# Performance work log

Hardware: AMD Instinct MI355X
Metric: run time of the kernel (lower is better)

## Reference

```python
import jax, jax.numpy as jnp
import numpy as np

GROUPS = 4
EPS = 1e-5


def conv1d(x, w, b):
    # x [B,Cin,NA,T], w [Cout,Cin,1,K], 'same' padding along T
    K = w.shape[-1]
    pad = (K - 1) // 2
    y = jax.lax.conv_general_dilated(x, w, (1, 1), [(0, 0), (pad, pad)],
                                     dimension_numbers=('NCHW', 'OIHW', 'NCHW'))
    return y + b[None, :, None, None]


def group_norm(x, g, b):
    B, C, H, W = x.shape
    xg = x.reshape(B, GROUPS, C // GROUPS, H, W)
    m = xg.mean((2, 3, 4), keepdims=True)
    v = xg.var((2, 3, 4), keepdims=True)
    xn = ((xg - m) * jax.lax.rsqrt(v + EPS)).reshape(B, C, H, W)
    return xn * g[None, :, None, None] + b[None, :, None, None]


def avg_pool_t(x, k):
    B, C, H, T = x.shape
    return x.reshape(B, C, H, T // k, k).mean(-1)


def branch(x, w1, b1, g1, be1, w2, b2, g2, be2):
    y = avg_pool_t(jax.nn.gelu(group_norm(conv1d(x, w1, b1), g1, be1), approximate=False), 2)
    y = avg_pool_t(jax.nn.gelu(group_norm(conv1d(y, w2, b2), g2, be2), approximate=False), 4)
    # B C NA T -> B NA (T C)
    B, C, NA, T = y.shape
    return jnp.transpose(y, (0, 2, 3, 1)).reshape(B, NA, T * C)


def rvq(feat, cbs):
    # feat [B,NA,D]; cbs [nq,V,D] -> residual vector quantization
    def step(res, cb):
        d = (res * res).sum(-1, keepdims=True) \
            - 2.0 * jnp.einsum('bnd,vd->bnv', res, cb) \
            + (cb * cb).sum(-1)              # [B,NA,V]
        idx = jnp.argmin(d, axis=-1)          # [B,NA]
        q = cb[idx]                           # gather [B,NA,D]
        return res - q, (q, idx)
    _, (qs, idxs) = jax.lax.scan(step, feat, cbs)
    return qs.sum(0), idxs                    # [B,NA,D], [nq,B,NA]


def reference(x, w11, w12, w13, w14, b1, g1, be1,
              w21, w22, w23, w24, b2, g2, be2, codebooks):
    B, N, A, T = x.shape
    xc = x.reshape(B, N * A, T)[:, None]  # [B,1,NA,T]
    feats = jnp.stack([
        branch(xc, w11, b1[0], g1[0], be1[0], w21, b2[0], g2[0], be2[0]),
        branch(xc, w12, b1[1], g1[1], be1[1], w22, b2[1], g2[1], be2[1]),
        branch(xc, w13, b1[2], g1[2], be1[2], w23, b2[2], g2[2], be2[2]),
        branch(xc, w14, b1[3], g1[3], be1[3], w24, b2[3], g2[3], be2[3]),
    ])  # [4,B,NA,D]
    quant, idxs = jax.vmap(rvq)(feats, codebooks)  # [4,B,NA,D], [4,nq,B,NA]
    # straight-through estimator
    out = feats + jax.lax.stop_gradient(quant - feats)
    return out, idxs


def setup_inputs() -> dict:
    key = jax.random.key(0)
    ks = jax.random.split(key, 16)
    C = 8
    d = {
        'x': jax.random.normal(ks[0], (8, 32, 4, 200), jnp.float32),
        'w11': jax.random.normal(ks[1], (C, 1, 1, 21), jnp.float32) * 0.1,
        'w12': jax.random.normal(ks[2], (C, 1, 1, 15), jnp.float32) * 0.1,
        'w13': jax.random.normal(ks[3], (C, 1, 1, 9), jnp.float32) * 0.1,
        'w14': jax.random.normal(ks[4], (C, 1, 1, 5), jnp.float32) * 0.1,
        'b1': jnp.zeros((4, C), jnp.float32),
        'g1': jnp.ones((4, C), jnp.float32),
        'be1': jnp.zeros((4, C), jnp.float32),
        'w21': jax.random.normal(ks[5], (C, C, 1, 9), jnp.float32) * 0.1,
        'w22': jax.random.normal(ks[6], (C, C, 1, 7), jnp.float32) * 0.1,
        'w23': jax.random.normal(ks[7], (C, C, 1, 5), jnp.float32) * 0.1,
        'w24': jax.random.normal(ks[8], (C, C, 1, 3), jnp.float32) * 0.1,
        'b2': jnp.zeros((4, C), jnp.float32),
        'g2': jnp.ones((4, C), jnp.float32),
        'be2': jnp.zeros((4, C), jnp.float32),
        'codebooks': jax.random.normal(ks[9], (4, 8, 8192, 200), jnp.float32) * 0.5,
    }
    return d
```

## Files before the change

kernel.cpp:

```cpp
#include <hip/hip_runtime.h>
#include <hip/hip_bf16.h>
#include <math.h>

#define NBR 4
#define BB 8
#define NAA 128
#define T_IN 200
#define CCH 8
#define NQ 8
#define NV 8192
#define DD 200
#define ROWS 1024
#define KPAD 224
#define NKG 28
#define CBQSH ((size_t)NBR*NKG*NV*8)

typedef __attribute__((ext_vector_type(8))) short short8;
typedef __attribute__((ext_vector_type(4))) float f32x4;

__device__ __forceinline__ unsigned short f2bf(float x) {
  unsigned u = __float_as_uint(x);
  unsigned r = (u + 0x7fffu + ((u >> 16) & 1u)) >> 16;
  return (unsigned short)r;
}
__device__ __forceinline__ bool lexlt(float av, int ai, float bv, int bi) {
  return (av < bv) || (av == bv && ai < bi);
}
__device__ __forceinline__ unsigned umn(unsigned a, unsigned b) { return a < b ? a : b; }
__device__ __forceinline__ unsigned umx(unsigned a, unsigned b) { return a > b ? a : b; }
__device__ __forceinline__ unsigned skey(float s, int idx) {
  unsigned u = __float_as_uint(s);
  unsigned mask = ((unsigned)((int)u >> 31)) | 0x80000000u;
  return ((u ^ mask) & 0xFFFFE000u) | (unsigned)idx;
}
__device__ __forceinline__ void gld16(const short* g, short* s) {
  __builtin_amdgcn_global_load_lds(
      (const __attribute__((address_space(1))) unsigned*)g,
      (__attribute__((address_space(3))) unsigned*)s, 16, 0, 0);
}

__device__ __forceinline__ void cvt_body(
    int cvtblk, int q0, const float* __restrict__ cbs,
    short* __restrict__ dh, float* __restrict__ cbn, short (*S)[65][8])
{
  const int vt = cvtblk & 127;
  const int t  = cvtblk >> 7;
  const int br = t >> 2, qr = t & 3;
  const int q = q0 + qr;
  const int tid = threadIdx.x;
  const int row = tid >> 2, fq = tid & 3;
  const int v0 = vt*64;
  const float* srow = cbs + ((size_t)(br*NQ + q)*NV + v0 + row)*DD;

  float s = 0.f;
  for (int j = 0; j < 13; ++j) {
    int f4 = fq + 4*j;
    if (f4 < 50) {
      float4 f = *(const float4*)&srow[4*f4];
      s += f.x*f.x + f.y*f.y + f.z*f.z + f.w*f.w;
      *(short4*)&S[f4>>1][row][(f4&1)*4] =
          make_short4((short)f2bf(f.x), (short)f2bf(f.y),
                      (short)f2bf(f.z), (short)f2bf(f.w));
    }
  }
  s += __shfl_xor(s, 1);
  s += __shfl_xor(s, 2);
  if (fq == 0) cbn[(size_t)(br*NQ + q)*NV + v0 + row] = s;
  __syncthreads();

  short* dq = dh + (size_t)q*CBQSH;
  for (int u = tid; u < NKG*64*2; u += 256) {
    int kg = u >> 7;
    int rem = u & 127;
    int v = rem >> 1, pos = (rem & 1)*4;
    short4 val = (kg < 25) ? *(const short4*)&S[kg][v][pos]
                           : make_short4(0,0,0,0);
    *(short4*)&dq[(((size_t)br*NKG + kg)*NV + v0 + v)*8 + pos] = val;
  }
}

template<int K>
__device__ __forceinline__ void conv1_stats_body(
    const float* __restrict__ sx, const float* __restrict__ wr, float bias,
    int tl, double& s, double& s2)
{
  constexpr int pad = (K-1)/2;
  if (tl < 25) {
    int t0 = 8*tl;
    float xw[K+7];
    #pragma unroll
    for (int i = 0; i < K+7; ++i) {
      int xi = t0 - pad + i;
      xw[i] = ((unsigned)xi < (unsigned)T_IN) ? sx[xi] : 0.f;
    }
    #pragma unroll
    for (int m = 0; m < 8; ++m) {
      float acc = bias;
      #pragma unroll
      for (int k = 0; k < K; ++k)
        acc = fmaf(wr[k], xw[m + k], acc);
      s += acc; s2 += (double)acc * acc;
    }
  }
}

__global__ __launch_bounds__(256) void k_front1(
    const float* __restrict__ x,
    const float* __restrict__ w11, const float* __restrict__ w12,
    const float* __restrict__ w13, const float* __restrict__ w14,
    const float* __restrict__ b1,
    double* __restrict__ partS, double* __restrict__ partQ,
    const float* __restrict__ cbs, short* __restrict__ dh,
    float* __restrict__ cbn)
{
  __shared__ float sx[T_IN];
  __shared__ double rs[256], rq[256];
  __shared__ short S[25][65][8];
  const int bid = blockIdx.x;
  const int tid = threadIdx.x;

  if (bid >= 4096) {
    cvt_body(bid - 4096, 0, cbs, dh, cbn, S);
    return;
  }

  const int br = bid >> 10;
  const int b  = (bid >> 7) & 7;
  const int na = bid & 127;
  const int c  = tid >> 5;
  const int tl = tid & 31;
  const float* w = (br==0) ? w11 : (br==1) ? w12 : (br==2) ? w13 : w14;

  if (tid < T_IN) sx[tid] = x[((size_t)b*NAA + na)*T_IN + tid];
  __syncthreads();

  const float bias = b1[br*CCH + c];
  double s = 0.0, s2 = 0.0;
  switch (br) {
    case 0: conv1_stats_body<21>(sx, w + c*21, bias, tl, s, s2); break;
    case 1: conv1_stats_body<15>(sx, w + c*15, bias, tl, s, s2); break;
    case 2: conv1_stats_body<9> (sx, w + c*9,  bias, tl, s, s2); break;
    default: conv1_stats_body<5>(sx, w + c*5,  bias, tl, s, s2); break;
  }
  rs[tid] = s; rq[tid] = s2;
  __syncthreads();
  for (int off = 32; off > 0; off >>= 1) {
    if ((tid & 63) < off) { rs[tid] += rs[tid+off]; rq[tid] += rq[tid+off]; }
    __syncthreads();
  }
  if ((tid & 63) == 0) {
    int g = tid >> 6;
    int pi = (((br*BB + b)*4 + g) << 7) + na;
    partS[pi] = rs[tid]; partQ[pi] = rq[tid];
  }
}

__global__ __launch_bounds__(256) void k_conv1_stats(
    const float* __restrict__ x,
    const float* __restrict__ w11, const float* __restrict__ w12,
    const float* __restrict__ w13, const float* __restrict__ w14,
    const float* __restrict__ b1,
    double* __restrict__ partS, double* __restrict__ partQ)
{
  const int bid = blockIdx.x;
  const int br = bid >> 10;
  const int b  = (bid >> 7) & 7;
  const int na = bid & 127;
  const int tid = threadIdx.x;
  const int c  = tid >> 5;
  const int tl = tid & 31;
  const float* w = (br==0) ? w11 : (br==1) ? w12 : (br==2) ? w13 : w14;

  __shared__ float sx[T_IN];
  if (tid < T_IN) sx[tid] = x[((size_t)b*NAA + na)*T_IN + tid];
  __syncthreads();

  const float bias = b1[br*CCH + c];
  double s = 0.0, s2 = 0.0;
  switch (br) {
    case 0: conv1_stats_body<21>(sx, w + c*21, bias, tl, s, s2); break;
    case 1: conv1_stats_body<15>(sx, w + c*15, bias, tl, s, s2); break;
    case 2: conv1_stats_body<9> (sx, w + c*9,  bias, tl, s, s2); break;
    default: conv1_stats_body<5>(sx, w + c*5,  bias, tl, s, s2); break;
  }
  __shared__ double rs[256], rq[256];
  rs[tid] = s; rq[tid] = s2;
  __syncthreads();
  for (int off = 32; off > 0; off >>= 1) {
    if ((tid & 63) < off) { rs[tid] += rs[tid+off]; rq[tid] += rq[tid+off]; }
    __syncthreads();
  }
  if ((tid & 63) == 0) {
    int g = tid >> 6;
    int pi = (((br*BB + b)*4 + g) << 7) + na;
    partS[pi] = rs[tid]; partQ[pi] = rq[tid];
  }
}

template<int K1, int K2>
__device__ __forceinline__ void mid_body(
    const float* __restrict__ sx, float* __restrict__ sy,
    const float* __restrict__ w1, const float* __restrict__ w2,
    float bias1, float fm, float rst, float gm, float bt, float bias2,
    int c, int tl, float* __restrict__ yout, double& s, double& s2)
{
  constexpr int pad1 = (K1-1)/2, pad2 = (K2-1)/2;
  const float* wr = w1 + c*K1;
  if (tl < 25) {
    int t0 = 8*tl;
    float xw[K1+7];
    #pragma unroll
    for (int i = 0; i < K1+7; ++i) {
      int xi = t0 - pad1 + i;
      xw[i] = ((unsigned)xi < (unsigned)T_IN) ? sx[xi] : 0.f;
    }
    #pragma unroll
    for (int m = 0; m < 4; ++m) {
      float u = 0.f;
      #pragma unroll
      for (int h = 0; h < 2; ++h) {
        float acc = bias1;
        #pragma unroll
        for (int k = 0; k < K1; ++k)
          acc = fmaf(wr[k], xw[2*m + h + k], acc);
        float xn = (acc - fm) * rst * gm + bt;
        u += 0.5f * xn * (1.0f + erff(xn * 0.70710678118654752440f));
      }
      sy[c*100 + 4*tl + m] = 0.5f * u;
    }
  }
  __syncthreads();
  if (tl < 25) {
    int t0 = 4*tl;
    float a0 = bias2, a1 = bias2, a2 = bias2, a3 = bias2;
    #pragma unroll
    for (int cin = 0; cin < CCH; ++cin) {
      const float* wr2 = w2 + (c*CCH + cin)*K2;
      float wv[K2];
      #pragma unroll
      for (int k = 0; k < K2; ++k) wv[k] = wr2[k];
      float yw[K2+3];
      #pragma unroll
      for (int i = 0; i < K2+3; ++i) {
        int yi = t0 - pad2 + i;
        yw[i] = ((unsigned)yi < 100u) ? sy[cin*100 + yi] : 0.f;
      }
      #pragma unroll
      for (int k = 0; k < K2; ++k) a0 = fmaf(wv[k], yw[k], a0);
      #pragma unroll
      for (int k = 0; k < K2; ++k) a1 = fmaf(wv[k], yw[1 + k], a1);
      #pragma unroll
      for (int k = 0; k < K2; ++k) a2 = fmaf(wv[k], yw[2 + k], a2);
      #pragma unroll
      for (int k = 0; k < K2; ++k) a3 = fmaf(wv[k], yw[3 + k], a3);
    }
    *(float4*)&yout[t0] = make_float4(a0, a1, a2, a3);
    s += a0; s2 += (double)a0 * a0;
    s += a1; s2 += (double)a1 * a1;
    s += a2; s2 += (double)a2 * a2;
    s += a3; s2 += (double)a3 * a3;
  }
}

__global__ __launch_bounds__(256) void k_mid(
    const float* __restrict__ x,
    const float* __restrict__ w11, const float* __restrict__ w12,
    const float* __restrict__ w13, const float* __restrict__ w14,
    const float* __restrict__ b1, const float* __restrict__ g1,
    const float* __restrict__ be1,
    const double* __restrict__ partS1, const double* __restrict__ partQ1,
    const float* __restrict__ w21, const float* __restrict__ w22,
    const float* __restrict__ w23, const float* __restrict__ w24,
    const float* __restrict__ b2,
    float* __restrict__ y2raw,
    double* __restrict__ partS, double* __restrict__ partQ,
    const float* __restrict__ cbs, short* __restrict__ dh,
    float* __restrict__ cbn)
{
  __shared__ float sx[T_IN];
  __shared__ float sy[CCH*100];
  __shared__ float sstat[8];
  __shared__ double rs[256], rq[256];
  __shared__ short S[25][65][8];

  const int bid = blockIdx.x;
  const int tid = threadIdx.x;

  if (bid >= 4096) {
    cvt_body(bid - 4096, 4, cbs, dh, cbn, S);
    return;
  }

  const int br = bid >> 10;
  const int b  = (bid >> 7) & 7;
  const int na = bid & 127;
  const int c  = tid >> 5;
  const int tl = tid & 31;
  const int wid = tid >> 6;
  const int l = tid & 63;
  const float* w1 = (br==0) ? w11 : (br==1) ? w12 : (br==2) ? w13 : w14;
  const float* w2 = (br==0) ? w21 : (br==1) ? w22 : (br==2) ? w23 : w24;

  if (tid < T_IN) sx[tid] = x[((size_t)b*NAA + na)*T_IN + tid];

  {
    int base = (((br*BB + b)*4 + wid) << 7);
    double a  = partS1[base + l] + partS1[base + 64 + l];
    double qn = partQ1[base + l] + partQ1[base + 64 + l];
    #pragma unroll
    for (int m = 32; m >= 1; m >>= 1) {
      a  += __shfl_xor(a, m);
      qn += __shfl_xor(qn, m);
    }
    if (l == 0) {
      double mean = a / 51200.0;
      double var  = qn / 51200.0 - mean*mean;
      sstat[wid*2]     = (float)mean;
      sstat[wid*2 + 1] = (float)(1.0 / sqrt(var + 1e-5));
    }
  }
  __syncthreads();

  const float bias1 = b1[br*CCH + c];
  const float fm  = sstat[(c>>1)*2];
  const float rst = sstat[(c>>1)*2 + 1];
  const float gm = g1[br*CCH + c], bt = be1[br*CCH + c];
  const float bias2 = b2[br*CCH + c];
  float* yout = y2raw + ((((size_t)br*BB + b)*CCH + c)*NAA + na)*100;

  double s = 0.0, s2 = 0.0;
  switch (br) {
    case 0: mid_body<21,9>(sx, sy, w1, w2, bias1, fm, rst, gm, bt, bias2, c, tl, yout, s, s2); break;
    case 1: mid_body<15,7>(sx, sy, w1, w2, bias1, fm, rst, gm, bt, bias2, c, tl, yout, s, s2); break;
    case 2: mid_body<9,5> (sx, sy, w1, w2, bias1, fm, rst, gm, bt, bias2, c, tl, yout, s, s2); break;
    default: mid_body<5,3>(sx, sy, w1, w2, bias1, fm, rst, gm, bt, bias2, c, tl, yout, s, s2); break;
  }

  rs[tid] = s; rq[tid] = s2;
  __syncthreads();
  for (int off = 32; off > 0; off >>= 1) {
    if ((tid & 63) < off) { rs[tid] += rs[tid+off]; rq[tid] += rq[tid+off]; }
    __syncthreads();
  }
  if ((tid & 63) == 0) {
    int g = tid >> 6;
    int pi = (((br*BB + b)*4 + g) << 7) + na;
    partS[pi] = rs[tid]; partQ[pi] = rq[tid];
  }
}

__global__ __launch_bounds__(256) void k_tail(
    const float* __restrict__ y2raw, const float* __restrict__ g2,
    const float* __restrict__ be2,
    const double* __restrict__ partS2, const double* __restrict__ partQ2,
    float* __restrict__ res, short* __restrict__ resh)
{
  const int tid = threadIdx.x;
  int idx = blockIdx.x * 256 + tid;
  int c  = idx & 7;
  int tp = (idx >> 3) % 25;
  int na = (idx / 200) & 127;
  int b  = (idx / 25600) & 7;
  int br = idx / 204800;
  const int wid = tid >> 6, l = tid & 63;

  if (idx < NBR*3*ROWS*8) {
    int pos = idx & 7;
    int prow = (idx >> 3) & 1023;
    int r2  = idx >> 13;
    int pbr = r2 / 3, kgp = r2 - pbr*3;
    resh[(((size_t)pbr*NKG + 25 + kgp)*ROWS + prow)*8 + pos] = 0;
  }

  __shared__ float sstat[8];
  {
    int base = (((br*BB + b)*4 + wid) << 7);
    double a  = partS2[base + l] + partS2[base + 64 + l];
    double qn = partQ2[base + l] + partQ2[base + 64 + l];
    #pragma unroll
    for (int m = 32; m >= 1; m >>= 1) {
      a  += __shfl_xor(a, m);
      qn += __shfl_xor(qn, m);
    }
    if (l == 0) {
      double mean = a / 25600.0;
      double var  = qn / 25600.0 - mean*mean;
      sstat[wid*2]     = (float)mean;
      sstat[wid*2 + 1] = (float)(1.0 / sqrt(var + 1e-5));
    }
  }
  __syncthreads();

  int g = c >> 1;
  float fm  = sstat[g*2];
  float rst = sstat[g*2 + 1];
  float gm = g2[br*CCH + c], bt = be2[br*CCH + c];
  float4 v = *(const float4*)&y2raw[((((size_t)br*BB + b)*CCH + c)*NAA + na)*100 + 4*tp];
  float sum4 = 0.f;
  #pragma unroll
  for (int h = 0; h < 4; ++h) {
    float xv = (h==0) ? v.x : (h==1) ? v.y : (h==2) ? v.z : v.w;
    float xn = (xv - fm) * rst * gm + bt;
    sum4 += 0.5f * xn * (1.0f + erff(xn * 0.70710678118654752440f));
  }
  float val = 0.25f * sum4;
  int row = b*NAA + na;
  res[((size_t)br*ROWS + row)*DD + tp*8 + c] = val;
  resh[(((size_t)br*NKG + tp)*ROWS + row)*8 + c] = (short)f2bf(val);
}

__global__ __launch_bounds__(256) void k_cvt_cb(
    const float* __restrict__ cbs, int q,
    short* __restrict__ dh, float* __restrict__ cbn)
{
  __shared__ short S[25][65][8];
  const int blk = blockIdx.x;
  const int vt = blk & 127;
  const int br = blk >> 7;
  const int tid = threadIdx.x;
  const int row = tid >> 2, fq = tid & 3;
  const int v0 = vt*64;
  const float* srow = cbs + ((size_t)(br*NQ + q)*NV + v0 + row)*DD;

  float s = 0.f;
  for (int j = 0; j < 13; ++j) {
    int f4 = fq + 4*j;
    if (f4 < 50) {
      float4 f = *(const float4*)&srow[4*f4];
      s += f.x*f.x + f.y*f.y + f.z*f.z + f.w*f.w;
      *(short4*)&S[f4>>1][row][(f4&1)*4] =
          make_short4((short)f2bf(f.x), (short)f2bf(f.y),
                      (short)f2bf(f.z), (short)f2bf(f.w));
    }
  }
  s += __shfl_xor(s, 1);
  s += __shfl_xor(s, 2);
  if (fq == 0) cbn[(size_t)(br*NQ + q)*NV + v0 + row] = s;
  __syncthreads();

  for (int u = tid; u < NKG*64*2; u += 256) {
    int kg = u >> 7;
    int rem = u & 127;
    int v = rem >> 1, pos = (rem & 1)*4;
    short4 val = (kg < 25) ? *(const short4*)&S[kg][v][pos]
                           : make_short4(0,0,0,0);
    *(short4*)&dh[(((size_t)br*NKG + kg)*NV + v0 + v)*8 + pos] = val;
  }
}

__global__ __launch_bounds__(256) void k_gemm(
    const short* __restrict__ resh, const short* __restrict__ cbh,
    const float* __restrict__ cbn, int q,
    unsigned* __restrict__ candk)
{
  __shared__ short S[2][4][130][8];

  const int p = blockIdx.x;
  const int x = p & 7;
  const int sIdx = p >> 3;
  const int br = sIdx >> 6;
  const int rb = (sIdx >> 3) & 7;
  const int vb = x*8 + (sIdx & 7);
  const int tid = threadIdx.x;
  const int w = tid >> 6;
  const int l = tid & 63;
  const int wr = w >> 1, wc = w & 1;
  const int kgl = l >> 4, fr = l & 15;

  f32x4 acc[4][4];
  #pragma unroll
  for (int i = 0; i < 4; ++i)
    #pragma unroll
    for (int j = 0; j < 4; ++j)
      acc[i][j] = (f32x4){0.f, 0.f, 0.f, 0.f};

  short8 aA[2][4];

  #define STAGE(nb, ks)                                                         \
    {                                                                           \
      _Pragma("unroll")                                                         \
      for (int i = 0; i < 4; ++i)                                               \
        aA[nb][i] = *(const short8*)&resh[                                      \
          (((size_t)br*NKG + (ks)*4 + kgl)*ROWS + rb*128 + wr*64 + i*16 + fr)*8]; \
      _Pragma("unroll")                                                         \
      for (int t = 0; t < 2; ++t) {                                             \
        int u = (w << 1) | t;                                                   \
        int kg = u >> 1, wh = u & 1;                                            \
        gld16(cbh + (((size_t)br*NKG + (ks)*4 + kg)*NV + vb*128 + wh*64 + l)*8, \
              &S[nb][kg][wh*64][0]);                                            \
      }                                                                         \
    }

  STAGE(0, 0);

  #pragma unroll
  for (int ks = 0; ks < 7; ++ks) {
    const int cur = ks & 1, nxt = cur ^ 1;
    if (ks < 6) {
      STAGE(nxt, ks + 1);
      asm volatile("s_waitcnt vmcnt(6)" ::: "memory");
    } else {
      asm volatile("s_waitcnt vmcnt(0)" ::: "memory");
    }
    __builtin_amdgcn_s_barrier();

    short8 bh[4];
    #pragma unroll
    for (int j = 0; j < 4; ++j)
      bh[j] = *(const short8*)&S[cur][kgl][wc*64 + j*16 + fr][0];
    #pragma unroll
    for (int i = 0; i < 4; ++i)
      #pragma unroll
      for (int j = 0; j < 4; ++j)
        acc[i][j] = __builtin_amdgcn_mfma_f32_16x16x32_bf16(aA[cur][i], bh[j], acc[i][j], 0, 0, 0);

    asm volatile("" ::: "memory");
    __builtin_amdgcn_s_barrier();
  }

  const float* cn = cbn + (size_t)(br*NQ + q)*NV;
  float nj[4]; int vgj[4];
  #pragma unroll
  for (int j = 0; j < 4; ++j) {
    vgj[j] = vb*128 + wc*64 + j*16 + fr;
    nj[j] = 0.5f * cn[vgj[j]];
  }
  #pragma unroll
  for (int i = 0; i < 4; ++i) {
    #pragma unroll
    for (int reg = 0; reg < 4; ++reg) {
      unsigned k0 = skey(nj[0] - acc[i][0][reg], vgj[0]);
      unsigned k1 = skey(nj[1] - acc[i][1][reg], vgj[1]);
      unsigned k2 = skey(nj[2] - acc[i][2][reg], vgj[2]);
      unsigned k3 = skey(nj[3] - acc[i][3][reg], vgj[3]);
      unsigned a = umn(k0, k1), b = umx(k0, k1);
      unsigned c = umn(k2, k3), d = umx(k2, k3);
      unsigned c1 = umn(a, c);
      unsigned c2 = umn(umx(a, c), umn(b, d));
      #pragma unroll
      for (int m = 1; m <= 8; m <<= 1) {
        unsigned o1 = __shfl_xor(c1, m);
        unsigned o2 = __shfl_xor(c2, m);
        unsigned t = umx(c1, o1);
        c1 = umn(c1, o1);
        c2 = umn(umn(t, c2), o2);
      }
      if (fr == 0) {
        int grow = br*ROWS + rb*128 + wr*64 + i*16 + kgl*4 + reg;
        size_t o = ((size_t)grow*64 + vb)*4 + wc*2;
        candk[o] = c1; candk[o+1] = c2;
      }
    }
  }
  #undef STAGE
}

__global__ __launch_bounds__(256) void k_update3(
    const float* __restrict__ cbs, const float* __restrict__ cbn,
    const unsigned* __restrict__ candk,
    float* __restrict__ res, float* __restrict__ outq,
    float* __restrict__ outi, short* __restrict__ resh, int q)
{
  const int wid = threadIdx.x >> 6;
  const int lane = threadIdx.x & 63;
  const int r = blockIdx.x*4 + wid;
  const int br = r >> 10;
  const int row = r & 1023;

  const unsigned* ck = candk + (size_t)r * 256;
  uint4 kk = *(const uint4*)&ck[4*lane];
  unsigned c0 = kk.x, c1 = kk.y, c2 = kk.z, c3 = kk.w;

  unsigned mykey = 0xFFFFFFFFu;
  #pragma unroll
  for (int t = 0; t < 8; ++t) {
    unsigned lm = umn(umn(c0, c1), umn(c2, c3));
    #pragma unroll
    for (int m = 1; m <= 32; m <<= 1)
      lm = umn(lm, __shfl_xor(lm, m));
    if (c0 == lm) c0 = 0xFFFFFFFFu;
    if (c1 == lm) c1 = 0xFFFFFFFFu;
    if (c2 == lm) c2 = 0xFFFFFFFFu;
    if (c3 == lm) c3 = 0xFFFFFFFFu;
    if ((lane >> 3) == t) mykey = lm;
  }
  const int mycand = (int)(mykey & 0x1FFFu);

  const int kl = lane & 7;
  const float* cbrow = cbs + ((size_t)(br*NQ + q)*NV + mycand)*DD;
  const float* rrow0 = res + (size_t)r*DD;
  float dot = 0.f;
  #pragma unroll
  for (int u = 0; u < 7; ++u) {
    int f4 = kl + 8*u;
    if (f4 < 50) {
      float4 r4 = *(const float4*)&rrow0[4*f4];
      float4 c4 = *(const float4*)&cbrow[4*f4];
      dot = fmaf(r4.x, c4.x, dot);
      dot = fmaf(r4.y, c4.y, dot);
      dot = fmaf(r4.z, c4.z, dot);
      dot = fmaf(r4.w, c4.w, dot);
    }
  }
  dot += __shfl_xor(dot, 1);
  dot += __shfl_xor(dot, 2);
  dot += __shfl_xor(dot, 4);
  float dist = fmaf(-2.f, dot, cbn[(size_t)(br*NQ + q)*NV + mycand]);

  float bv = dist; int bi = mycand;
  #pragma unroll
  for (int m = 8; m <= 32; m <<= 1) {
    float ov = __shfl_xor(bv, m); int oi = __shfl_xor(bi, m);
    if (lexlt(ov, oi, bv, bi)) { bv = ov; bi = oi; }
  }

  if (lane == 0)
    outi[(((size_t)br*NQ + q)*BB + (row >> 7))*NAA + (row & 127)] = (float)bi;

  const float* c = cbs + ((size_t)(br*NQ + q)*NV + bi)*DD;
  float* rrow = res  + ((size_t)br*ROWS + row)*DD;
  float* qrow = outq + ((size_t)br*ROWS + row)*DD;
  if (lane < 50) {
    float4 cvv = *(const float4*)&c[4*lane];
    float4 r4 = *(const float4*)&rrow[4*lane];
    r4.x -= cvv.x; r4.y -= cvv.y; r4.z -= cvv.z; r4.w -= cvv.w;
    *(float4*)&rrow[4*lane] = r4;
    float4 qv;
    if (q == 0) {
      qv = cvv;
    } else {
      qv = *(const float4*)&qrow[4*lane];
      qv.x += cvv.x; qv.y += cvv.y; qv.z += cvv.z; qv.w += cvv.w;
    }
    *(float4*)&qrow[4*lane] = qv;

    *(short4*)&resh[(((size_t)br*NKG + (lane>>1))*ROWS + row)*8 + (lane&1)*4] =
        make_short4((short)f2bf(r4.x), (short)f2bf(r4.y),
                    (short)f2bf(r4.z), (short)f2bf(r4.w));
  }
}

extern "C" void kernel_launch(void* const* d_in, const int* in_sizes, int n_in,
                              void* d_out, int out_size, void* d_ws, size_t ws_size,
                              hipStream_t stream)
{
  const float* x   = (const float*)d_in[0];
  const float* w11 = (const float*)d_in[1];
  const float* w12 = (const float*)d_in[2];
  const float* w13 = (const float*)d_in[3];
  const float* w14 = (const float*)d_in[4];
  const float* b1  = (const float*)d_in[5];
  const float* g1  = (const float*)d_in[6];
  const float* be1 = (const float*)d_in[7];
  const float* w21 = (const float*)d_in[8];
  const float* w22 = (const float*)d_in[9];
  const float* w23 = (const float*)d_in[10];
  const float* w24 = (const float*)d_in[11];
  const float* b2  = (const float*)d_in[12];
  const float* g2  = (const float*)d_in[13];
  const float* be2 = (const float*)d_in[14];
  const float* cbs = (const float*)d_in[15];

  char* wsb = (char*)d_ws;
  double* partS1 = (double*)wsb;
  double* partQ1 = partS1 + 16384;
  double* partS2 = partQ1 + 16384;
  double* partQ2 = partS2 + 16384;
  float* fbase = (float*)(partQ2 + 16384);
  float* y2raw = fbase;
  float* res   = y2raw + 3276800;
  float* cbn   = res + 819200;
  unsigned* candk = (unsigned*)(cbn + 262144);
  short* resh  = (short*)(candk + 1048576);
  short* cbh   = resh + 917504;
  const size_t base_bytes = (char*)cbh - wsb;
  const bool big = ws_size >= base_bytes + CBQSH*8*sizeof(short) + 1024;

  float* outq = (float*)d_out;
  float* outi = outq + 819200;

  if (big) {
    k_front1<<<4096 + 2048, 256, 0, stream>>>(x, w11, w12, w13, w14, b1,
                                              partS1, partQ1, cbs, cbh, cbn);
    k_mid<<<4096 + 2048, 256, 0, stream>>>(x, w11, w12, w13, w14, b1, g1, be1,
                                           partS1, partQ1,
                                           w21, w22, w23, w24, b2, y2raw,
                                           partS2, partQ2, cbs, cbh, cbn);
  } else {
    k_conv1_stats<<<4096, 256, 0, stream>>>(x, w11, w12, w13, w14, b1, partS1, partQ1);
    k_mid<<<4096, 256, 0, stream>>>(x, w11, w12, w13, w14, b1, g1, be1,
                                    partS1, partQ1,
                                    w21, w22, w23, w24, b2, y2raw,
                                    partS2, partQ2, cbs, cbh, cbn);
  }
  k_tail<<<3200, 256, 0, stream>>>(y2raw, g2, be2, partS2, partQ2, res, resh);

  for (int q = 0; q < NQ; ++q) {
    if (!big)
      k_cvt_cb<<<NBR*128, 256, 0, stream>>>(cbs, q, cbh, cbn);
    const short* cbh_q = cbh + (big ? (size_t)q*CBQSH : 0);
    k_gemm<<<2048, 256, 0, stream>>>(resh, cbh_q, cbn, q, candk);
    k_update3<<<1024, 256, 0, stream>>>(cbs, cbn, candk, res, outq, outi, resh, q);
  }
}
```

Measured before the change: 427.3 us.

## Fuse RVQ gemm/update loop into one persistent cooperative kernel with grid sync

Replaces the 16 per-stage kernel launches (gemm plus update for each of 8 quantizer levels) with a single persistent cooperative kernel of 512 blocks. Each block loops over 4 gemm tiles and 2 update rows per level, separated by grid-wide syncs. The aim is to remove launch overhead and inter-kernel gaps. In exchange it limits parallelism to 512 blocks (2 per CU), adds two grid barriers per level, and falls back to the old path if cooperative launch is unavailable.

```diff
diff --git a/kernel.cpp b/kernel.cpp
--- a/kernel.cpp
+++ b/kernel.cpp
@@ -1,6 +1,9 @@
 #include <hip/hip_runtime.h>
+#include <hip/hip_cooperative_groups.h>
 #include <hip/hip_bf16.h>
 #include <math.h>
+
+namespace cg = cooperative_groups;
 
 #define NBR 4
 #define BB 8
@@ -11,7 +14,6 @@
 #define NV 8192
 #define DD 200
 #define ROWS 1024
-#define KPAD 224
 #define NKG 28
 #define CBQSH ((size_t)NBR*NKG*NV*8)
 
@@ -448,14 +450,11 @@
   }
 }
 
-__global__ __launch_bounds__(256) void k_gemm(
-    const short* __restrict__ resh, const short* __restrict__ cbh,
-    const float* __restrict__ cbn, int q,
-    unsigned* __restrict__ candk)
-{
-  __shared__ short S[2][4][130][8];
-
-  const int p = blockIdx.x;
+__device__ __forceinline__ void gemm_tile(
+    int p, const short* __restrict__ resh, const short* __restrict__ cbh_q,
+    const float* __restrict__ cbn_q4, int q, unsigned* __restrict__ candk,
+    short (*S)[4][130][8])
+{
   const int x = p & 7;
   const int sIdx = p >> 3;
   const int br = sIdx >> 6;
@@ -476,19 +475,19 @@
 
   short8 aA[2][4];
 
-  #define STAGE(nb, ks)                                                         \
-    {                                                                           \
-      _Pragma("unroll")                                                         \
-      for (int i = 0; i < 4; ++i)                                               \
-        aA[nb][i] = *(const short8*)&resh[                                      \
+  #define STAGE(nb, ks)                                                           \
+    {                                                                             \
+      _Pragma("unroll")                                                           \
+      for (int i = 0; i < 4; ++i)                                                 \
+        aA[nb][i] = *(const short8*)&resh[                                        \
           (((size_t)br*NKG + (ks)*4 + kgl)*ROWS + rb*128 + wr*64 + i*16 + fr)*8]; \
-      _Pragma("unroll")                                                         \
-      for (int t = 0; t < 2; ++t) {                                             \
-        int u = (w << 1) | t;                                                   \
-        int kg = u >> 1, wh = u & 1;                                            \
-        gld16(cbh + (((size_t)br*NKG + (ks)*4 + kg)*NV + vb*128 + wh*64 + l)*8, \
-              &S[nb][kg][wh*64][0]);                                            \
-      }                                                                         \
+      _Pragma("unroll")                                                           \
+      for (int t = 0; t < 2; ++t) {                                               \
+        int u = (w << 1) | t;                                                     \
+        int kg = u >> 1, wh = u & 1;                                              \
+        gld16(cbh_q + (((size_t)br*NKG + (ks)*4 + kg)*NV + vb*128 + wh*64 + l)*8, \
+              &S[nb][kg][wh*64][0]);                                              \
+      }                                                                           \
     }
 
   STAGE(0, 0);
@@ -517,8 +516,9 @@
     asm volatile("" ::: "memory");
     __builtin_amdgcn_s_barrier();
   }
-
-  const float* cn = cbn + (size_t)(br*NQ + q)*NV;
+  #undef STAGE
+
+  const float* cn = cbn_q4 + (size_t)(br*NQ + q)*NV;
   float nj[4]; int vgj[4];
   #pragma unroll
   for (int j = 0; j < 4; ++j) {
@@ -552,18 +552,14 @@
       }
     }
   }
-  #undef STAGE
-}
-
-__global__ __launch_bounds__(256) void k_update3(
-    const float* __restrict__ cbs, const float* __restrict__ cbn,
-    const unsigned* __restrict__ candk,
-    float* __restrict__ res, float* __restrict__ outq,
-    float* __restrict__ outi, short* __restrict__ resh, int q)
-{
-  const int wid = threadIdx.x >> 6;
-  const int lane = threadIdx.x & 63;
-  const int r = blockIdx.x*4 + wid;
+}
+
+__device__ __forceinline__ void update_row(
+    int r, const float* __restrict__ cbs, const float* __restrict__ cbn,
+    const unsigned* __restrict__ candk, float* __restrict__ res,
+    float* __restrict__ outq, float* __restrict__ outi,
+    short* __restrict__ resh, int q, int lane)
+{
   const int br = r >> 10;
   const int row = r & 1023;
 
@@ -637,6 +633,54 @@
     *(short4*)&resh[(((size_t)br*NKG + (lane>>1))*ROWS + row)*8 + (lane&1)*4] =
         make_short4((short)f2bf(r4.x), (short)f2bf(r4.y),
                     (short)f2bf(r4.z), (short)f2bf(r4.w));
+  }
+}
+
+__global__ __launch_bounds__(256) void k_gemm(
+    const short* __restrict__ resh, const short* __restrict__ cbh,
+    const float* __restrict__ cbn, int q,
+    unsigned* __restrict__ candk)
+{
+  __shared__ short S[2][4][130][8];
+  gemm_tile(blockIdx.x, resh, cbh, cbn - (size_t)0, q, candk, S);
+}
+
+__global__ __launch_bounds__(256) void k_update3(
+    const float* __restrict__ cbs, const float* __restrict__ cbn,
+    const unsigned* __restrict__ candk,
+    float* __restrict__ res, float* __restrict__ outq,
+    float* __restrict__ outi, short* __restrict__ resh, int q)
+{
+  const int wid = threadIdx.x >> 6;
+  const int lane = threadIdx.x & 63;
+  update_row(blockIdx.x*4 + wid, cbs, cbn, candk, res, outq, outi, resh, q, lane);
+}
+
+__global__ __launch_bounds__(256, 2) void k_rvq(
+    short* resh, const short* cbh, const float* cbn, unsigned* candk,
+    const float* cbs, float* res, float* outq, float* outi)
+{
+  cg::grid_group grid = cg::this_grid();
+  __shared__ short S[2][4][130][8];
+  const int wid = threadIdx.x >> 6;
+  const int lane = threadIdx.x & 63;
+
+  for (int q = 0; q < NQ; ++q) {
+    const short* cbh_q = cbh + (size_t)q*CBQSH;
+    #pragma unroll 1
+    for (int t = 0; t < 4; ++t)
+      gemm_tile((int)blockIdx.x + 512*t, resh, cbh_q, cbn, q, candk, S);
+
+    __threadfence();
+    grid.sync();
+
+    #pragma unroll 1
+    for (int rr = 0; rr < 2; ++rr)
+      update_row((int)blockIdx.x*8 + wid*2 + rr, cbs, cbn, candk,
+                 res, outq, outi, resh, q, lane);
+
+    __threadfence();
+    grid.sync();
   }
 }
 
@@ -695,11 +739,29 @@
   }
   k_tail<<<3200, 256, 0, stream>>>(y2raw, g2, be2, partS2, partQ2, res, resh);
 
-  for (int q = 0; q < NQ; ++q) {
-    if (!big)
-      k_cvt_cb<<<NBR*128, 256, 0, stream>>>(cbs, q, cbh, cbn);
-    const short* cbh_q = cbh + (big ? (size_t)q*CBQSH : 0);
-    k_gemm<<<2048, 256, 0, stream>>>(resh, cbh_q, cbn, q, candk);
-    k_update3<<<1024, 256, 0, stream>>>(cbs, cbn, candk, res, outq, outi, resh, q);
-  }
-}
+  bool coop = false;
+  if (big) {
+    int dev = 0; hipGetDevice(&dev);
+    int attr = 0;
+    hipDeviceGetAttribute(&attr, hipDeviceAttributeCooperativeLaunch, dev);
+    int nb = 0;
+    hipOccupancyMaxActiveBlocksPerMultiprocessor(&nb, (const void*)k_rvq, 256, 0);
+    if (attr && nb >= 2) {
+      void* args[] = {(void*)&resh, (void*)&cbh, (void*)&cbn, (void*)&candk,
+                      (void*)&cbs, (void*)&res, (void*)&outq, (void*)&outi};
+      hipError_t e = hipLaunchCooperativeKernel((const void*)k_rvq, dim3(512),
+                                                dim3(256), args, 0, stream);
+      coop = (e == hipSuccess);
+    }
+  }
+
+  if (!coop) {
+    for (int q = 0; q < NQ; ++q) {
+      if (!big)
+        k_cvt_cb<<<NBR*128, 256, 0, stream>>>(cbs, q, cbh, cbn);
+      const short* cbh_q = cbh + (big ? (size_t)q*CBQSH : 0);
+      k_gemm<<<2048, 256, 0, stream>>>(resh, cbh_q, cbn, q, candk);
+      k_update3<<<1024, 256, 0, stream>>>(cbs, cbn, candk, res, outq, outi, resh, q);
+    }
+  }
+}
```

Measured after the change: 429.1 us. Within noise of the previous version (+0.4%).
